# Performance work log

Hardware: AMD Instinct MI355X
Metric: run time of the kernel (lower is better)

The kernel has to match this reference:

```python
import jax, jax.numpy as jnp
import numpy as np

H = 16  # num_heads

def _rotate_half(x):
    x1, x2 = jnp.split(x, 2, axis=-1)
    return jnp.concatenate((-x2, x1), axis=-1)

def setup_inputs() -> dict:
    key = jax.random.key(0)
    ks = jax.random.split(key, 8)
    B, N, C = 4, 2048, 1024
    d = C // H
    x = jax.random.normal(ks[0], (B, N, C), dtype=jnp.float32)
    cos = jax.random.uniform(ks[1], (1, 1, N, d), dtype=jnp.float32)
    sin = jax.random.uniform(ks[2], (1, 1, N, d), dtype=jnp.float32)
    s = 0.02
    Wq = jax.random.normal(ks[3], (C, C), dtype=jnp.float32) * s
    Wkv = jax.random.normal(ks[4], (C, 2 * C), dtype=jnp.float32) * s
    Wout = jax.random.normal(ks[5], (C, C), dtype=jnp.float32) * s
    bout = jnp.zeros((C,), dtype=jnp.float32)
    return {"x": x, "cos": cos, "sin": sin, "Wq": Wq, "Wkv": Wkv, "Wout": Wout, "bout": bout}

def reference(x, cos, sin, Wq, Wkv, Wout, bout):
    B, N, C = x.shape
    d = C // H
    scale = d ** (-0.5)
    # projections (qkv_bias=False)
    q = (x @ Wq).reshape(B, N, H, d).transpose(0, 2, 1, 3)        # (B,H,N,d)
    kv = x @ Wkv                                                   # (B,N,2C)
    k, v = jnp.split(kv, 2, axis=-1)
    k = k.reshape(B, N, H, d).transpose(0, 2, 1, 3)
    v = v.reshape(B, N, H, d).transpose(0, 2, 1, 3)
    # inline RoPE
    q = q * cos + _rotate_half(q) * sin
    k = k * cos + _rotate_half(k) * sin
    # naive full attention
    sim = jnp.einsum('bhid,bhjd->bhij', q, k) * scale              # (B,H,N,N)
    attn = jax.nn.softmax(sim, axis=-1)
    out = jnp.einsum('bhij,bhjd->bhid', attn, v)                   # (B,H,N,d)
    out = out.transpose(0, 2, 1, 3).reshape(B, N, C)
    return out @ Wout + bout
```

## Files before the change

### kernel.cpp

```cpp
#include <hip/hip_runtime.h>


typedef unsigned short u16;
typedef unsigned int u32;
typedef __attribute__((ext_vector_type(4))) short s16x4;
typedef __attribute__((ext_vector_type(8))) short short8;
typedef __attribute__((ext_vector_type(8))) unsigned short ushort8;
typedef __attribute__((ext_vector_type(4))) float f32x4;

#define MFMA16x16x32 __builtin_amdgcn_mfma_f32_16x16x32_bf16
#define QSCALE 0.180336880434135f

#if __has_builtin(__builtin_amdgcn_exp2f)
#define EXP2F __builtin_amdgcn_exp2f
#else
#define EXP2F exp2f
#endif

__device__ __forceinline__ float b2f(u16 u) {
  union { u32 i; float f; } x; x.i = ((u32)u) << 16; return x.f;
}
__device__ __forceinline__ u16 f2b(float f) {
  union { float f; u32 i; } x; x.f = f;
  u32 r = (x.i + 0x7FFFu + ((x.i >> 16) & 1u)) >> 16;
  return (u16)r;
}
__device__ __forceinline__ u32 f2b_trunc32(float f) {
  union { float f; u32 i; } x; x.f = f;
  return x.i >> 16;
}
__device__ __forceinline__ bool detect_f32(const u32* __restrict__ cw) {
  u32 acc = 0;
#pragma unroll
  for (int i = 0; i < 64; ++i) acc |= cw[i];
  return (acc & 0x8000u) != 0;
}
__device__ __forceinline__ float ldval(const void* p, long i, bool f32) {
  return f32 ? ((const float*)p)[i] : b2f(((const u16*)p)[i]);
}
__device__ __forceinline__ ushort8 ld8f(const float* p) {
  float4 u0 = *(const float4*)p;
  float4 u1 = *(const float4*)(p + 4);
  ushort8 r;
  r[0] = f2b(u0.x); r[1] = f2b(u0.y); r[2] = f2b(u0.z); r[3] = f2b(u0.w);
  r[4] = f2b(u1.x); r[5] = f2b(u1.y); r[6] = f2b(u1.z); r[7] = f2b(u1.w);
  return r;
}
__device__ __forceinline__ void async16(const void* g, void* l) {
  __builtin_amdgcn_global_load_lds((const __attribute__((address_space(1))) void*)g,
                                   (__attribute__((address_space(3))) void*)l, 16, 0, 0);
}

__global__ __launch_bounds__(256)
void convert_x(const void* __restrict__ src, u16* __restrict__ dst,
               const u32* __restrict__ cosw) {
  const bool f32 = detect_f32(cosw);
  const long i = ((long)blockIdx.x * 256 + threadIdx.x) * 8;
  ushort8 v;
  if (f32) v = ld8f((const float*)src + i);
  else     v = *(const ushort8*)((const u16*)src + i);
  *(ushort8*)(dst + i) = v;
}

__global__ __launch_bounds__(256)
void transpose_any(const void* __restrict__ src, u16* __restrict__ dst,
                   int R, int C, const u32* __restrict__ cosw) {
  const bool f32 = detect_f32(cosw);
  const int tr = blockIdx.y * 64, tc = blockIdx.x * 64;
  __shared__ __align__(16) u16 tile[64][65];
  const int t = threadIdx.x;
#pragma unroll
  for (int i = 0; i < 2; ++i) {
    const int ch = i * 256 + t;
    const int r = ch >> 3, cc = ch & 7;
    ushort8 v;
    if (f32) v = ld8f((const float*)src + (long)(tr + r) * C + tc + cc * 8);
    else     v = *(const ushort8*)((const u16*)src + (long)(tr + r) * C + tc + cc * 8);
#pragma unroll
    for (int j = 0; j < 8; ++j) tile[r][cc * 8 + j] = v[j];
  }
  __syncthreads();
#pragma unroll
  for (int i = 0; i < 2; ++i) {
    const int ch = i * 256 + t;
    const int c = ch >> 3, rc = ch & 7;
    ushort8 v;
#pragma unroll
    for (int j = 0; j < 8; ++j) v[j] = tile[rc * 8 + j][c];
    *(ushort8*)(dst + (long)(tc + c) * R + tr + rc * 8) = v;
  }
}

__global__ __launch_bounds__(256)
void transpose_b16(const u16* __restrict__ src, u16* __restrict__ dst,
                   int R, int C, long sb, long db) {
  src += (long)blockIdx.z * sb;
  dst += (long)blockIdx.z * db;
  const int tr = blockIdx.y * 64, tc = blockIdx.x * 64;
  __shared__ __align__(16) u16 tile[64][65];
  const int t = threadIdx.x;
#pragma unroll
  for (int i = 0; i < 2; ++i) {
    const int ch = i * 256 + t;
    const int r = ch >> 3, cc = ch & 7;
    ushort8 v = *(const ushort8*)(src + (long)(tr + r) * C + tc + cc * 8);
#pragma unroll
    for (int j = 0; j < 8; ++j) tile[r][cc * 8 + j] = v[j];
  }
  __syncthreads();
#pragma unroll
  for (int i = 0; i < 2; ++i) {
    const int ch = i * 256 + t;
    const int c = ch >> 3, rc = ch & 7;
    ushort8 v;
#pragma unroll
    for (int j = 0; j < 8; ++j) v[j] = tile[rc * 8 + j][c];
    *(ushort8*)(dst + (long)(tc + c) * R + tr + rc * 8) = v;
  }
}

template <int MODE>
__global__ __launch_bounds__(256)
void gemm_fast(const u16* __restrict__ A, const u16* __restrict__ BT,
               const void* cosp, const void* sinp,
               u16* q_ws, u16* k_ws, u16* v_ws,
               const void* bias, void* outp, const u32* __restrict__ cosw) {
  constexpr int K = 1024, ITERS = K / 32;
  __shared__ __align__(16) u16 As[2][128 * 32];
  __shared__ __align__(16) u16 Bs[2][128 * 32];
  const int tid = threadIdx.x;
  const int wave = tid >> 6, lane = tid & 63;
  const int quad = lane >> 4, l15 = lane & 15;
  const int m0 = blockIdx.y * 128, n0 = blockIdx.x * 128;
  const int mh = (wave >> 1) * 64, nh = (wave & 1) * 64;
  const f32x4 zero4 = {0.f, 0.f, 0.f, 0.f};

  f32x4 acc[4][4];
#pragma unroll
  for (int i = 0; i < 4; ++i)
#pragma unroll
    for (int j = 0; j < 4; ++j) acc[i][j] = zero4;

  const int c0 = tid, c1 = 256 + tid;
  const u16* a0p = A  + (long)(m0 + (c0 >> 2)) * K + (c0 & 3) * 8;
  const u16* a1p = A  + (long)(m0 + (c1 >> 2)) * K + (c1 & 3) * 8;
  const u16* b0p = BT + (long)(n0 + (c0 >> 2)) * K + (c0 & 3) * 8;
  const u16* b1p = BT + (long)(n0 + (c1 >> 2)) * K + (c1 & 3) * 8;

#define STAGE(buf, kt)                                \
  do {                                                \
    async16(a0p + (kt), As[buf] + c0 * 8);            \
    async16(a1p + (kt), As[buf] + c1 * 8);            \
    async16(b0p + (kt), Bs[buf] + c0 * 8);            \
    async16(b1p + (kt), Bs[buf] + c1 * 8);            \
  } while (0)

  STAGE(0, 0);
  for (int it = 0; it < ITERS; ++it) {
    const int cur = it & 1;
    __syncthreads();
    if (it + 1 < ITERS) STAGE(cur ^ 1, (it + 1) * 32);
    short8 af[4], bf[4];
#pragma unroll
    for (int s = 0; s < 4; ++s) {
      af[s] = *(const short8*)(As[cur] + (mh + s * 16 + l15) * 32 + quad * 8);
      bf[s] = *(const short8*)(Bs[cur] + (nh + s * 16 + l15) * 32 + quad * 8);
    }
#pragma unroll
    for (int i = 0; i < 4; ++i)
#pragma unroll
      for (int j = 0; j < 4; ++j)
        acc[i][j] = MFMA16x16x32(af[i], bf[j], acc[i][j], 0, 0, 0);
  }
#undef STAGE

  const bool f32 = detect_f32(cosw);

  if (MODE == 0) {
    const int seg = n0 >> 10;
    const int csbase = (n0 & 1023) + nh;
    u16* segp = (seg == 0) ? q_ws : (seg == 1) ? k_ws : v_ws;
#pragma unroll
    for (int i = 0; i < 4; ++i) {
#pragma unroll
      for (int r = 0; r < 4; ++r) {
        const int mm = m0 + mh + i * 16 + quad * 4 + r;
        const int b = mm >> 11, n = mm & 2047;
#pragma unroll
        for (int j = 0; j < 4; ++j) {
          const int cs = csbase + j * 16 + l15;
          const int h = cs >> 6, dv = cs & 63;
          float val = acc[i][j][r];
          if (seg < 2) {
            const float cv = ldval(cosp, (long)n * 64 + dv, f32);
            const float sv = ldval(sinp, (long)n * 64 + dv, f32);
            const float part = acc[i][j ^ 2][r];
            val = val * cv + ((dv < 32) ? -part : part) * sv;
            if (seg == 0) val *= QSCALE;
          }
          segp[(((long)(b * 16 + h) * 2048 + n) << 6) + dv] = f2b(val);
        }
      }
    }
  } else {
#pragma unroll
    for (int i = 0; i < 4; ++i) {
#pragma unroll
      for (int r = 0; r < 4; ++r) {
        const int mm = m0 + mh + i * 16 + quad * 4 + r;
#pragma unroll
        for (int j = 0; j < 4; ++j) {
          const int cc = n0 + nh + j * 16 + l15;
          const float val = acc[i][j][r] + ldval(bias, cc, f32);
          if (f32) ((float*)outp)[(long)mm * 1024 + cc] = val;
          else     ((u16*)outp)[(long)mm * 1024 + cc] = f2b(val);
        }
      }
    }
  }
}

__global__ __launch_bounds__(512, 4)
void flash_k(const u16* __restrict__ q_ws, const u16* __restrict__ k_ws,
             const u16* __restrict__ vT_ws, u16* __restrict__ attn) {
  __shared__ __align__(16) u16 Ks[2][64 * 64];
  __shared__ __align__(16) u16 Vts[2][64 * 64];
  const int tid = threadIdx.x, wave = tid >> 6, lane = tid & 63;
  const int quad = lane >> 4, l15 = lane & 15;
  const int s7 = l15 & 7;
  const int bid = blockIdx.x + (blockIdx.y << 3);
  const int qx = bid >> 6;
  const int bh = ((bid & 7) << 3) | ((bid >> 3) & 7);
  const int qr0 = qx * 256 + wave * 32;
  const u16* Q  = q_ws  + (long)bh * 2048 * 64;
  const u16* Kp = k_ws  + (long)bh * 2048 * 64;
  const u16* Vt = vT_ws + (long)bh * 64 * 2048;
  const f32x4 zero4 = {0.f, 0.f, 0.f, 0.f};
  short8 ones;
#pragma unroll
  for (int i = 0; i < 8; ++i) ones[i] = (short)0x3F80;

  short8 aq[2][2];
#pragma unroll
  for (int ms = 0; ms < 2; ++ms)
#pragma unroll
    for (int ks = 0; ks < 2; ++ks)
      aq[ms][ks] = *(const short8*)(Q + (long)(qr0 + ms * 16 + l15) * 64 + ks * 32 + quad * 8);

  f32x4 accO[2][4], accL[2];
#pragma unroll
  for (int ms = 0; ms < 2; ++ms) {
#pragma unroll
    for (int jd = 0; jd < 4; ++jd) accO[ms][jd] = zero4;
    accL[ms] = zero4;
  }

  const int rr = tid >> 3, gg = ((tid & 7) ^ (rr & 7)) * 8;

#define STAGEKV(buf, kt)                                          \
  do {                                                            \
    async16(Kp + (long)((kt) + rr) * 64 + gg, Ks[buf] + tid * 8); \
    async16(Vt + (long)rr * 2048 + (kt) + gg, Vts[buf] + tid * 8);\
  } while (0)

  const int vh = (quad & 1) * 4;
  const int vc0a = ((0 + (quad >> 1)) ^ s7) * 8 + vh;
  const int vc0b = ((2 + (quad >> 1)) ^ s7) * 8 + vh;
  const int vc1a = ((4 + (quad >> 1)) ^ s7) * 8 + vh;
  const int vc1b = ((6 + (quad >> 1)) ^ s7) * 8 + vh;

  STAGEKV(0, 0);
  for (int it = 0; it < 32; ++it) {
    const int cur = it & 1;
    __syncthreads();
    if (it + 1 < 32) STAGEKV(cur ^ 1, (it + 1) * 64);

#pragma unroll
    for (int k2 = 0; k2 < 2; ++k2) {
      u32 pk[2][4];
#pragma unroll
      for (int nsl = 0; nsl < 2; ++nsl) {
        const int ns = k2 * 2 + nsl;
        const u16* rowK = Ks[cur] + (ns * 16 + l15) * 64;
        short8 b0 = *(const short8*)(rowK + ((quad ^ s7) * 8));
        short8 b1 = *(const short8*)(rowK + (((quad + 4) ^ s7) * 8));
#pragma unroll
        for (int ms = 0; ms < 2; ++ms) {
          f32x4 t = MFMA16x16x32(b0, aq[ms][0], zero4, 0, 0, 0);
          f32x4 sa = MFMA16x16x32(b1, aq[ms][1], t, 0, 0, 0);
          const u32 p0 = f2b_trunc32(EXP2F(sa[0]));
          const u32 p1 = f2b_trunc32(EXP2F(sa[1]));
          const u32 p2 = f2b_trunc32(EXP2F(sa[2]));
          const u32 p3 = f2b_trunc32(EXP2F(sa[3]));
          pk[ms][nsl * 2 + 0] = p0 | (p1 << 16);
          pk[ms][nsl * 2 + 1] = p2 | (p3 << 16);
        }
      }
      short8 ap[2];
#pragma unroll
      for (int ms = 0; ms < 2; ++ms) {
        union { u32 w[4]; short8 s; } u;
        u.w[0] = pk[ms][0]; u.w[1] = pk[ms][1];
        u.w[2] = pk[ms][2]; u.w[3] = pk[ms][3];
        ap[ms] = u.s;
        accL[ms] = MFMA16x16x32(ap[ms], ones, accL[ms], 0, 0, 0);
      }
      const int ca = k2 ? vc1a : vc0a;
      const int cb = k2 ? vc1b : vc0b;
#pragma unroll
      for (int jd = 0; jd < 4; ++jd) {
        const u16* rowV = Vts[cur] + (jd * 16 + l15) * 64;
        union { s16x4 h[2]; short8 s; } bv;
        bv.h[0] = *(const s16x4*)(rowV + ca);
        bv.h[1] = *(const s16x4*)(rowV + cb);
#pragma unroll
        for (int ms = 0; ms < 2; ++ms)
          accO[ms][jd] = MFMA16x16x32(ap[ms], bv.s, accO[ms][jd], 0, 0, 0);
      }
    }
  }
#undef STAGEKV

  const int b = bh >> 4, h = bh & 15;
#pragma unroll
  for (int ms = 0; ms < 2; ++ms) {
#pragma unroll
    for (int r = 0; r < 4; ++r) {
      const float inv = 1.f / accL[ms][r];
      const int row = qr0 + ms * 16 + quad * 4 + r;
#pragma unroll
      for (int jd = 0; jd < 4; ++jd) {
        const int cc = h * 64 + jd * 16 + l15;
        attn[((long)(b * 2048 + row)) * 1024 + cc] = f2b(accO[ms][jd][r] * inv);
      }
    }
  }
}

extern "C" void kernel_launch(void* const* d_in, const int* in_sizes, int n_in,
                              void* d_out, int out_size, void* d_ws, size_t ws_size,
                              hipStream_t stream) {
  const void* x    = d_in[0];
  const void* cosp = d_in[1];
  const void* sinp = d_in[2];
  const void* Wq   = d_in[3];
  const void* Wkv  = d_in[4];
  const void* Wout = d_in[5];
  const void* bout = d_in[6];
  const u32* cosw  = (const u32*)d_in[1];

  char* ws = (char*)d_ws;
  const size_t MB = 1u << 20;
  u16* q_ws  = (u16*)(ws);
  u16* k_ws  = (u16*)(ws + 16 * MB);
  u16* vT_ws = (u16*)(ws + 32 * MB);
  u16* v_ws  = (u16*)(ws + 48 * MB);
  u16* attn  = (u16*)(ws + 48 * MB);
  u16* WoutT = (u16*)(ws + 32 * MB);

  u16* WT1;
  if (ws_size >= 88 * MB) WT1 = (u16*)(ws + 64 * MB);
  else                    WT1 = (u16*)d_out;
  u16* x_bf16 = WT1 + 3072 * 1024;

  convert_x<<<dim3(4096), 256, 0, stream>>>(x, x_bf16, cosw);
  transpose_any<<<dim3(16, 16), 256, 0, stream>>>(Wq, WT1, 1024, 1024, cosw);
  transpose_any<<<dim3(32, 16), 256, 0, stream>>>(Wkv, WT1 + 1024 * 1024, 1024, 2048, cosw);
  gemm_fast<0><<<dim3(24, 64), 256, 0, stream>>>(x_bf16, WT1, cosp, sinp,
                                                 q_ws, k_ws, v_ws,
                                                 nullptr, nullptr, cosw);
  transpose_b16<<<dim3(1, 32, 64), 256, 0, stream>>>(v_ws, vT_ws, 2048, 64,
                                                     (long)2048 * 64, (long)64 * 2048);
  flash_k<<<dim3(8, 64), 512, 0, stream>>>(q_ws, k_ws, vT_ws, attn);
  transpose_any<<<dim3(16, 16), 256, 0, stream>>>(Wout, WoutT, 1024, 1024, cosw);
  gemm_fast<1><<<dim3(8, 64), 256, 0, stream>>>(attn, WoutT, cosp, sinp,
                                                nullptr, nullptr, nullptr,
                                                bout, d_out, cosw);
}
```

Measured before the change: 329.7 us.

## Double GEMM K-tile to 64 with XOR-swizzled shared memory layout

The projection GEMM now stages 64-wide K slices per iteration instead of 32, halving the number of barrier-separated iterations. Shared-memory rows are XOR-swizzled by row index so that 16-byte fragment reads avoid bank conflicts on the wider 128-byte rows. This doubles the LDS footprint to 64KB per block, which may reduce occupancy.

```diff
diff --git a/kernel.cpp b/kernel.cpp
--- a/kernel.cpp
+++ b/kernel.cpp
@@ -125,12 +125,13 @@
                const void* cosp, const void* sinp,
                u16* q_ws, u16* k_ws, u16* v_ws,
                const void* bias, void* outp, const u32* __restrict__ cosw) {
-  constexpr int K = 1024, ITERS = K / 32;
-  __shared__ __align__(16) u16 As[2][128 * 32];
-  __shared__ __align__(16) u16 Bs[2][128 * 32];
+  constexpr int K = 1024, ITERS = K / 64;
+  __shared__ __align__(16) u16 As[2][128 * 64];
+  __shared__ __align__(16) u16 Bs[2][128 * 64];
   const int tid = threadIdx.x;
   const int wave = tid >> 6, lane = tid & 63;
   const int quad = lane >> 4, l15 = lane & 15;
+  const int s7 = l15 & 7;
   const int m0 = blockIdx.y * 128, n0 = blockIdx.x * 128;
   const int mh = (wave >> 1) * 64, nh = (wave & 1) * 64;
   const f32x4 zero4 = {0.f, 0.f, 0.f, 0.f};
@@ -141,30 +142,40 @@
 #pragma unroll
     for (int j = 0; j < 4; ++j) acc[i][j] = zero4;
 
-  const int c0 = tid, c1 = 256 + tid;
-  const u16* a0p = A  + (long)(m0 + (c0 >> 2)) * K + (c0 & 3) * 8;
-  const u16* a1p = A  + (long)(m0 + (c1 >> 2)) * K + (c1 & 3) * 8;
-  const u16* b0p = BT + (long)(n0 + (c0 >> 2)) * K + (c0 & 3) * 8;
-  const u16* b1p = BT + (long)(n0 + (c1 >> 2)) * K + (c1 & 3) * 8;
-
-#define STAGE(buf, kt)                                \
-  do {                                                \
-    async16(a0p + (kt), As[buf] + c0 * 8);            \
-    async16(a1p + (kt), As[buf] + c1 * 8);            \
-    async16(b0p + (kt), Bs[buf] + c0 * 8);            \
-    async16(b1p + (kt), Bs[buf] + c1 * 8);            \
+  const int srow = tid >> 3;
+  const int scg = ((tid & 7) ^ (srow & 7)) * 8;
+  const u16* Asrc = A  + (long)(m0 + srow) * K + scg;
+  const u16* Bsrc = BT + (long)(n0 + srow) * K + scg;
+
+#define STAGE(buf, kt)                                                  \
+  do {                                                                  \
+    _Pragma("unroll")                                                   \
+    for (int p = 0; p < 4; ++p) {                                       \
+      async16(Asrc + (long)p * 32 * K + (kt), As[buf] + (p * 256 + tid) * 8); \
+      async16(Bsrc + (long)p * 32 * K + (kt), Bs[buf] + (p * 256 + tid) * 8); \
+    }                                                                   \
   } while (0)
 
   STAGE(0, 0);
   for (int it = 0; it < ITERS; ++it) {
     const int cur = it & 1;
     __syncthreads();
-    if (it + 1 < ITERS) STAGE(cur ^ 1, (it + 1) * 32);
+    if (it + 1 < ITERS) STAGE(cur ^ 1, (it + 1) * 64);
     short8 af[4], bf[4];
 #pragma unroll
     for (int s = 0; s < 4; ++s) {
-      af[s] = *(const short8*)(As[cur] + (mh + s * 16 + l15) * 32 + quad * 8);
-      bf[s] = *(const short8*)(Bs[cur] + (nh + s * 16 + l15) * 32 + quad * 8);
+      af[s] = *(const short8*)(As[cur] + (mh + s * 16 + l15) * 64 + ((quad ^ s7) * 8));
+      bf[s] = *(const short8*)(Bs[cur] + (nh + s * 16 + l15) * 64 + ((quad ^ s7) * 8));
+    }
+#pragma unroll
+    for (int i = 0; i < 4; ++i)
+#pragma unroll
+      for (int j = 0; j < 4; ++j)
+        acc[i][j] = MFMA16x16x32(af[i], bf[j], acc[i][j], 0, 0, 0);
+#pragma unroll
+    for (int s = 0; s < 4; ++s) {
+      af[s] = *(const short8*)(As[cur] + (mh + s * 16 + l15) * 64 + (((4 + quad) ^ s7) * 8));
+      bf[s] = *(const short8*)(Bs[cur] + (nh + s * 16 + l15) * 64 + (((4 + quad) ^ s7) * 8));
     }
 #pragma unroll
     for (int i = 0; i < 4; ++i)
```

After: 328.6 us. No clear change (-0.3%).
